# Kernel optimization log

Hardware: AMD Instinct MI355X
Metric: run time of the kernel (lower is better)

## Reference

```python
import jax, jax.numpy as jnp
from jax import lax
import numpy as np

EMBED, HIDDEN, VOCAB = 512, 512, 10000
ATT, ENC = 512, 2048
B, NPIX, T = 128, 49, 30


def _lin(k, out_d, in_d):
    k1, k2 = jax.random.split(k)
    s = 1.0 / np.sqrt(in_d)
    return (jax.random.uniform(k1, (out_d, in_d), minval=-s, maxval=s),
            jax.random.uniform(k2, (out_d,), minval=-s, maxval=s))


def setup_inputs() -> dict:
    key = jax.random.key(0)
    ks = jax.random.split(key, 24)
    inp = {}
    inp['enc_image'] = jax.random.normal(ks[0], (B, NPIX, ENC))
    inp['global_features'] = jax.random.normal(ks[1], (B, ENC))
    inp['encoded_captions'] = jax.random.randint(ks[2], (B, T), 0, VOCAB)
    lens = jax.random.randint(ks[3], (B,), 1, T + 1).at[0].set(T)
    inp['caption_lengths'] = lens[:, None]
    # parameters
    inp['emb_W'] = jax.random.uniform(ks[4], (VOCAB, EMBED), minval=-0.1, maxval=0.1)
    inp['e2h_W'], inp['e2h_b'] = _lin(ks[5], HIDDEN, ENC)
    inp['gf_W'], inp['gf_b'] = _lin(ks[6], EMBED, ENC)
    inp['fc_W'] = jax.random.uniform(ks[7], (VOCAB, HIDDEN), minval=-0.1, maxval=0.1)
    inp['fc_b'] = jnp.zeros((VOCAB,))
    inp['lstm_Wih'], inp['lstm_bih'] = _lin(ks[8], 4 * HIDDEN, 2 * EMBED)
    inp['lstm_Whh'], inp['lstm_bhh'] = _lin(ks[9], 4 * HIDDEN, HIDDEN)
    inp['xg_W'], inp['xg_b'] = _lin(ks[10], HIDDEN, 2 * EMBED)
    inp['hg_W'], inp['hg_b'] = _lin(ks[11], HIDDEN, HIDDEN)
    inp['senaff_W'], inp['senaff_b'] = _lin(ks[12], HIDDEN, HIDDEN)
    inp['senatt_W'], inp['senatt_b'] = _lin(ks[13], ATT, HIDDEN)
    inp['haff_W'], inp['haff_b'] = _lin(ks[14], HIDDEN, HIDDEN)
    inp['hatt_W'], inp['hatt_b'] = _lin(ks[15], ATT, HIDDEN)
    inp['vatt_W'], inp['vatt_b'] = _lin(ks[16], ATT, HIDDEN)
    inp['alph_W'], inp['alph_b'] = _lin(ks[17], 1, ATT)
    inp['ctx_W'], inp['ctx_b'] = _lin(ks[18], HIDDEN, HIDDEN)
    return inp


def reference(enc_image, global_features, encoded_captions, caption_lengths,
              emb_W, e2h_W, e2h_b, gf_W, gf_b, fc_W, fc_b,
              lstm_Wih, lstm_bih, lstm_Whh, lstm_bhh,
              xg_W, xg_b, hg_W, hg_b,
              senaff_W, senaff_b, senatt_W, senatt_b,
              haff_W, haff_b, hatt_W, hatt_b,
              vatt_W, vatt_b, alph_W, alph_b, ctx_W, ctx_b):
    lengths = caption_lengths[:, 0]
    order = jnp.argsort(-lengths)                     # descending (stable)
    lengths = lengths[order]
    spatial = jax.nn.relu(jnp.einsum('bpe,he->bph', enc_image[order], e2h_W) + e2h_b)  # (B,NP,H)
    gimg = jax.nn.relu(global_features[order] @ gf_W.T + gf_b)                          # (B,E)
    embs = emb_W[encoded_captions[order]]                                               # (B,T,E)
    inputs = jnp.concatenate([embs, jnp.broadcast_to(gimg[:, None, :], embs.shape)], axis=-1)  # (B,T,2E)
    vattn = jnp.einsum('bph,ah->bpa', spatial, vatt_W) + vatt_b                         # (B,NP,A) hoisted
    h0 = jnp.zeros((spatial.shape[0], HIDDEN), spatial.dtype)
    c0 = h0

    def step(carry, xs):
        h, c = carry
        xt, mask = xs                                  # (B,2E), (B,) bool = row still active
        gates = xt @ lstm_Wih.T + lstm_bih + h @ lstm_Whh.T + lstm_bhh
        i, f, g, o = jnp.split(gates, 4, axis=-1)
        c_new = jax.nn.sigmoid(f) * c + jax.nn.sigmoid(i) * jnp.tanh(g)
        h_new = jax.nn.sigmoid(o) * jnp.tanh(c_new)
        st = jax.nn.sigmoid(xt @ xg_W.T + xg_b + h @ hg_W.T + hg_b) * jnp.tanh(c_new)  # sentinel
        sen_aff = jax.nn.relu(st @ senaff_W.T + senaff_b)    # (B,H)
        sen_att = sen_aff @ senatt_W.T + senatt_b            # (B,A)
        h_aff = jnp.tanh(h_new @ haff_W.T + haff_b)
        h_att = h_aff @ hatt_W.T + hatt_b
        att_feats = jnp.concatenate([vattn, sen_att[:, None, :]], axis=1)   # (B,NP+1,A)
        scores = jnp.tanh(att_feats + h_att[:, None, :]) @ alph_W[0] + alph_b[0]
        alpha = jax.nn.softmax(scores, axis=1)               # (B,NP+1)
        cat_feats = jnp.concatenate([spatial, sen_aff[:, None, :]], axis=1)
        context = jnp.einsum('bph,bp->bh', cat_feats, alpha)
        out_l = jnp.tanh((context + h_aff) @ ctx_W.T + ctx_b)
        pt = out_l @ fc_W.T + fc_b                           # dropout = identity (eval)
        m = mask[:, None]
        return (jnp.where(m, h_new, h), jnp.where(m, c_new, c)), jnp.where(m, pt, 0.0)

    masks = lengths[None, :] > jnp.arange(T)[:, None]        # (T,B) replicates shrinking batch_size_t
    _, preds = lax.scan(step, (h0, c0), (jnp.swapaxes(inputs, 0, 1), masks))
    return jnp.swapaxes(preds, 0, 1)                         # (B,T,VOCAB), sorted-by-length order
```

## Files before the change

### kernel.cpp

```cpp
#include <hip/hip_runtime.h>
#include <hip/hip_bf16.h>
#include <cstdint>
#include <cstddef>

#define DEVI __device__ __forceinline__

#define BB 128
#define TT 30
#define VOCAB 10000
#define ENCD 2048
#define NPIX 49
#define SLOT 65536

typedef __attribute__((ext_vector_type(8))) short bf16x8;
typedef __attribute__((ext_vector_type(4))) float f32x4;

DEVI float bf2f(unsigned short u){ union{float f; unsigned int i;} x; x.i=((unsigned)u)<<16; return x.f; }
DEVI unsigned short f2bf(float f){ union{float f; unsigned int i;} x; x.f=f; unsigned r=x.i + 0x7fffu + ((x.i>>16)&1u); return (unsigned short)(r>>16); }
DEVI float sigm(float x){ return 1.0f/(1.0f+expf(-x)); }
DEVI f32x4 mfma16(bf16x8 a, bf16x8 b, f32x4 c){ return __builtin_amdgcn_mfma_f32_16x16x32_bf16(a,b,c,0,0,0); }

DEVI void gload_lds16(const void* g, void* l){
  __builtin_amdgcn_global_load_lds((const __attribute__((address_space(1))) unsigned int*)g,
                                   (__attribute__((address_space(3))) unsigned int*)l, 16, 0, 0);
}

DEVI void waitarr(int* base, int n, int thresh){
  __syncthreads();
  if(threadIdx.x < 64){
    for(;;){
      int v = (threadIdx.x<n) ? __hip_atomic_load(base + threadIdx.x*16, __ATOMIC_RELAXED, __HIP_MEMORY_SCOPE_AGENT)
                              : 0x7fffffff;
      if(__all(v >= thresh)) break;
      __builtin_amdgcn_s_sleep(8);
    }
  }
  asm volatile("" ::: "memory");
  __syncthreads();
}
DEVI void setflag(int* f, int val){
  __syncthreads();
  if(threadIdx.x==0) __hip_atomic_store(f, val, __ATOMIC_RELEASE, __HIP_MEMORY_SCOPE_AGENT);
}

__global__ void k_sort(const int* __restrict__ lens, int* __restrict__ order, int* __restrict__ Bt){
  __shared__ int L[BB];
  int i = threadIdx.x;
  L[i] = lens[i];
  __syncthreads();
  int li = L[i]; int rank = 0;
  for(int j=0;j<BB;j++){ int lj=L[j]; rank += (lj>li) || (lj==li && j<i); }
  order[rank] = i;
  if(i<TT){ int c=0; for(int j=0;j<BB;j++) c += (L[j]>i); Bt[i]=c; }
}

struct WC13 { const float* src[13]; unsigned short* dst[13]; int n[13]; };
__global__ void k_wconv(WC13 wc){
  int stride = gridDim.x*blockDim.x;
  int tid0 = blockIdx.x*blockDim.x + threadIdx.x;
  for(int s=0;s<13;s++){
    const float4* src=(const float4*)wc.src[s];
    int n4 = wc.n[s]>>2;
    ushort4* dst=(ushort4*)wc.dst[s];
    for(int i=tid0;i<n4;i+=stride){
      float4 v=src[i];
      ushort4 o; o.x=f2bf(v.x); o.y=f2bf(v.y); o.z=f2bf(v.z); o.w=f2bf(v.w);
      dst[i]=o;
    }
  }
}

__global__ void k_xt(const int* __restrict__ caps, const int* __restrict__ order,
                     const float* __restrict__ embW, const unsigned short* __restrict__ gimg,
                     unsigned short* __restrict__ xt){
  int total=BB*TT*1024;
  for(int idx=blockIdx.x*blockDim.x+threadIdx.x; idx<total; idx+=gridDim.x*blockDim.x){
    int k=idx&1023; int bt=idx>>10; int t=bt%TT; int b=bt/TT;
    unsigned short v;
    if(k<512){ int tok=caps[order[b]*TT+t]; v=f2bf(embW[(size_t)tok*512+k]); }
    else v=gimg[b*512+(k-512)];
    xt[idx]=v;
  }
}

__global__ __launch_bounds__(256) void k_gemm_f32A2(
    const float* __restrict__ A, int lda, int rpb, const int* __restrict__ order,
    const unsigned short* __restrict__ W, const float* __restrict__ bias,
    unsigned short* __restrict__ out, int K)
{
  __shared__ unsigned short As[128][136];
  int tid=threadIdx.x, wave=tid>>6, lane=tid&63, l15=lane&15, l4=lane>>4;
  int mb = blockIdx.y*128;
  f32x4 acc[8][4];
  f32x4 z = {0.f,0.f,0.f,0.f};
  #pragma unroll
  for(int i=0;i<8;i++)
    #pragma unroll
    for(int j=0;j<4;j++) acc[i][j]=z;
  int cch=tid&15, r0=tid>>4;
  int nb = blockIdx.x*256 + wave*64;
  for(int kc=0;kc<K;kc+=128){
    __syncthreads();
    #pragma unroll
    for(int rp=0;rp<8;rp++){
      int r=r0+rp*16;
      int m=mb+r;
      int sb = order[m/rpb]*rpb + m%rpb;
      const float* p = A + (size_t)sb*lda + kc + cch*8;
      float4 v0=*(const float4*)p, v1=*(const float4*)(p+4);
      unsigned short* d=&As[r][cch*8];
      d[0]=f2bf(v0.x); d[1]=f2bf(v0.y); d[2]=f2bf(v0.z); d[3]=f2bf(v0.w);
      d[4]=f2bf(v1.x); d[5]=f2bf(v1.y); d[6]=f2bf(v1.z); d[7]=f2bf(v1.w);
    }
    __syncthreads();
    #pragma unroll
    for(int kk=0;kk<4;kk++){
      bf16x8 bfr[4];
      #pragma unroll
      for(int nt=0;nt<4;nt++)
        bfr[nt] = *(const bf16x8*)(W + (size_t)(nb+nt*16+l15)*K + kc + kk*32 + l4*8);
      #pragma unroll
      for(int mt=0;mt<8;mt++){
        bf16x8 af = *(const bf16x8*)&As[mt*16+l15][kk*32+l4*8];
        #pragma unroll
        for(int nt=0;nt<4;nt++) acc[mt][nt]=mfma16(af,bfr[nt],acc[mt][nt]);
      }
    }
  }
  #pragma unroll
  for(int nt=0;nt<4;nt++){
    int n = nb + nt*16 + l15;
    float bs = bias[n];
    #pragma unroll
    for(int mt=0;mt<8;mt++){
      #pragma unroll
      for(int j=0;j<4;j++){
        int row = mb + mt*16 + l4*4 + j;
        float v = acc[mt][nt][j]+bs; v = v>0.f ? v : 0.f;
        out[(size_t)row*512 + n] = f2bf(v);
      }
    }
  }
}

DEVI void dev_gemm512c(unsigned short (*As)[136], const unsigned short* A, const unsigned short* W,
                       const float* bias, unsigned short* out, int xtile){
  int tid=threadIdx.x, wave=tid>>6, lane=tid&63, l15=lane&15, l4=lane>>4;
  f32x4 acc[8];
  f32x4 z = {0.f,0.f,0.f,0.f};
  #pragma unroll
  for(int i=0;i<8;i++) acc[i]=z;
  int cch=tid&15, r0=tid>>4;
  int nrow = xtile*64 + wave*16 + l15;
  for(int kc=0;kc<512;kc+=128){
    __syncthreads();
    #pragma unroll
    for(int rp=0;rp<8;rp++){
      int r=r0+rp*16;
      *(uint4*)&As[r][cch*8] = *(const uint4*)(A + (size_t)r*512 + kc + cch*8);
    }
    __syncthreads();
    #pragma unroll
    for(int kk=0;kk<4;kk++){
      bf16x8 bfr = *(const bf16x8*)(W + (size_t)nrow*512 + kc + kk*32 + l4*8);
      #pragma unroll
      for(int mt=0;mt<8;mt++){
        bf16x8 af = *(const bf16x8*)&As[mt*16+l15][kk*32+l4*8];
        acc[mt]=mfma16(af,bfr,acc[mt]);
      }
    }
  }
  float bs = bias ? bias[nrow] : 0.f;
  #pragma unroll
  for(int mt=0;mt<8;mt++){
    #pragma unroll
    for(int j=0;j<4;j++){
      int row = mt*16 + l4*4 + j;
      out[(size_t)row*512+nrow]=f2bf(acc[mt][j]+bs);
    }
  }
  __syncthreads();
}

struct PreD { const unsigned short* A; const unsigned short* W; const float* bias; unsigned short* out; };
struct PreD2 { PreD d[2]; };
__global__ __launch_bounds__(256) void k_pre(PreD2 dd){
  __shared__ unsigned short As[128][136];
  PreD g = dd.d[blockIdx.z];
  dev_gemm512c(As, g.A + (size_t)blockIdx.y*128*512, g.W, g.bias,
               g.out + (size_t)blockIdx.y*128*512, blockIdx.x);
}

__global__ __launch_bounds__(256) void k_gx(
    const unsigned short* __restrict__ xt, const unsigned short* __restrict__ w_ih,
    const unsigned short* __restrict__ w_xg,
    const float* __restrict__ bih, const float* __restrict__ bhh,
    const float* __restrict__ bxg, const float* __restrict__ bhg,
    unsigned short* __restrict__ Gx)
{
  __shared__ unsigned short As[128][136];
  int tid=threadIdx.x, wave=tid>>6, lane=tid&63, l15=lane&15, l4=lane>>4;
  int t = blockIdx.y;
  f32x4 acc[8];
  f32x4 z = {0.f,0.f,0.f,0.f};
  #pragma unroll
  for(int i=0;i<8;i++) acc[i]=z;
  int cch=tid&15, r0=tid>>4;
  int n = blockIdx.x*64 + wave*16 + l15;
  const unsigned short* wrow = (n<2048) ? (w_ih + (size_t)n*1024) : (w_xg + (size_t)(n-2048)*1024);
  for(int kc=0;kc<1024;kc+=128){
    __syncthreads();
    #pragma unroll
    for(int rp=0;rp<8;rp++){
      int r=r0+rp*16;
      *(uint4*)&As[r][cch*8] = *(const uint4*)(xt + (size_t)r*(TT*1024) + t*1024 + kc + cch*8);
    }
    __syncthreads();
    #pragma unroll
    for(int kk=0;kk<4;kk++){
      bf16x8 bfr = *(const bf16x8*)(wrow + kc + kk*32 + l4*8);
      #pragma unroll
      for(int mt=0;mt<8;mt++){
        bf16x8 af = *(const bf16x8*)&As[mt*16+l15][kk*32+l4*8];
        acc[mt]=mfma16(af,bfr,acc[mt]);
      }
    }
  }
  float bias = (n<2048) ? (bih[n]+bhh[n]) : (bxg[n-2048]+bhg[n-2048]);
  #pragma unroll
  for(int mt=0;mt<8;mt++){
    int row = mt*16 + l4*4;
    ushort4 o;
    o.x=f2bf(acc[mt][0]+bias); o.y=f2bf(acc[mt][1]+bias);
    o.z=f2bf(acc[mt][2]+bias); o.w=f2bf(acc[mt][3]+bias);
    *(ushort4*)(Gx + ((size_t)t*2560 + n)*128 + row) = o;
  }
}

struct PCtx {
  const unsigned short *w_hh, *w_hg, *Gx;
  const unsigned short *w_saff, *w_satt, *w_haff, *w_hatt, *w_ctx, *w_fc;
  const unsigned short *vattn, *SC;
  const float *sab,*stbias,*hab,*htb, *alW,*alb, *cxb, *fcb;
  const int *Bt;
  unsigned short *h_hist;
  unsigned short *stb;
  unsigned short *sbuf;
  float *dout;
  int *Lf,*SAf,*SBf,*S3f;
};

DEVI void stage_async(char* lds, const unsigned short* src){
  int wave = threadIdx.x>>6, lane = threadIdx.x&63;
  #pragma unroll
  for(int i=0;i<32;i++){
    int row = wave*32 + i;
    const unsigned short* g = src + (size_t)row*512 + ((lane ^ (row&7))<<3);
    gload_lds16(g, lds + row*1024 + lane*16);
  }
}
DEVI bf16x8 ldsA(const char* lds, int R, int cb){
  return *(const bf16x8*)(lds + R*1024 + (((unsigned)cb<<1) ^ ((unsigned)(R&7)<<4)));
}

DEVI void dev_lstmP(char* lds, const PCtx& p, int t, int cb,
                    const unsigned short* hprev, unsigned short* hout, float creg[2][4]){
  int tid=threadIdx.x, wave=tid>>6, lane=tid&63, l15=lane&15, l4=lane>>4;
  int jb = cb*16;
  int bt = p.Bt[t];
  __syncthreads();
  if(t>0) stage_async(lds, hprev);
  f32x4 acc[2][5];
  #pragma unroll
  for(int m=0;m<2;m++){
    #pragma unroll
    for(int s=0;s<5;s++){
      int col = (s<4) ? (s*512 + jb + l15) : (2048 + jb + l15);
      int row = (wave*2+m)*16 + l4*4;
      ushort4 g = *(const ushort4*)(p.Gx + ((size_t)t*2560 + col)*128 + row);
      acc[m][s][0]=bf2f(g.x); acc[m][s][1]=bf2f(g.y); acc[m][s][2]=bf2f(g.z); acc[m][s][3]=bf2f(g.w);
    }
  }
  __syncthreads();
  if(t>0){
    #pragma unroll
    for(int kk=0;kk<16;kk++){
      int kg = kk*32 + l4*8;
      bf16x8 bfr[5];
      #pragma unroll
      for(int s=0;s<5;s++){
        const unsigned short* wp = (s<4) ? (p.w_hh + (size_t)(s*512+jb+l15)*512 + kg)
                                         : (p.w_hg + (size_t)(jb+l15)*512 + kg);
        bfr[s] = *(const bf16x8*)wp;
      }
      #pragma unroll
      for(int m=0;m<2;m++){
        bf16x8 af = ldsA(lds, (wave*2+m)*16+l15, kk*32+l4*8);
        #pragma unroll
        for(int s=0;s<5;s++) acc[m][s]=mfma16(af,bfr[s],acc[m][s]);
      }
    }
  }
  int j = jb + l15;
  unsigned short* stt = p.stb + (size_t)t*SLOT;
  #pragma unroll
  for(int m=0;m<2;m++){
    int mt = wave*2+m;
    #pragma unroll
    for(int jj=0;jj<4;jj++){
      int b = mt*16 + l4*4 + jj;
      float iv = sigm(acc[m][0][jj]);
      float fv = sigm(acc[m][1][jj]);
      float gv = tanhf(acc[m][2][jj]);
      float ov = sigm(acc[m][3][jj]);
      float sv = sigm(acc[m][4][jj]);
      float cn = fv*creg[m][jj] + iv*gv;
      float tc = tanhf(cn);
      int hw = f2bf(ov*tc);
      int sw = f2bf(sv*tc);
      int hp = __shfl_xor(hw,1);
      int sp = __shfl_xor(sw,1);
      if(b<bt){
        if((l15&1)==0){
          *(unsigned*)(hout + (size_t)b*512 + j) = (unsigned)(hw&0xffff) | ((unsigned)hp<<16);
          *(unsigned*)(stt  + (size_t)b*512 + j) = (unsigned)(sw&0xffff) | ((unsigned)sp<<16);
        }
        creg[m][jj]=cn;
      }
    }
  }
}

DEVI void dev_mm1(char* lds, const unsigned short* src, const unsigned short* W,
                  const float* bias, unsigned short* out, int act, int xtile, int bt){
  int tid=threadIdx.x, wave=tid>>6, lane=tid&63, l15=lane&15, l4=lane>>4;
  __syncthreads();
  stage_async(lds, src);
  __syncthreads();
  int nrow = xtile*64 + wave*16 + l15;
  f32x4 acc[8];
  f32x4 z = {0.f,0.f,0.f,0.f};
  #pragma unroll
  for(int i=0;i<8;i++) acc[i]=z;
  #pragma unroll
  for(int kk=0;kk<16;kk++){
    bf16x8 bfr = *(const bf16x8*)(W + (size_t)nrow*512 + kk*32 + l4*8);
    #pragma unroll
    for(int mt=0;mt<8;mt++){
      bf16x8 af = ldsA(lds, mt*16+l15, kk*32+l4*8);
      acc[mt]=mfma16(af,bfr,acc[mt]);
    }
  }
  float bs = bias ? bias[nrow] : 0.f;
  #pragma unroll
  for(int mt=0;mt<8;mt++){
    #pragma unroll
    for(int j=0;j<4;j++){
      float v = acc[mt][j]+bs;
      if(act==1) v = fmaxf(v,0.f);
      else if(act==2) v = tanhf(v);
      int w = f2bf(v);
      int pw = __shfl_xor(w,1);
      int row = mt*16 + l4*4 + j;
      if((l15&1)==0 && row<bt)
        *(unsigned*)(out + (size_t)row*512 + (nrow&~1)) = (unsigned)(w&0xffff) | ((unsigned)pw<<16);
    }
  }
}

DEVI void dev_attn(float* sS, float* sA, unsigned short* sHA, unsigned short* sSA,
                   int b, const PCtx& p,
                   const unsigned short* satt, const unsigned short* hatt,
                   const unsigned short* scs, const unsigned short* sch,
                   unsigned short* outl){
  int tid=threadIdx.x;
  if(tid<64)       *(uint4*)&sHA[tid*8] = *(const uint4*)(hatt + (size_t)b*512 + tid*8);
  else if(tid<128){ int q=tid-64; *(uint4*)&sSA[q*8] = *(const uint4*)(satt + (size_t)b*512 + q*8); }
  __syncthreads();
  int gid=tid>>4, gl=tid&15;
  #pragma unroll
  for(int rp=0;rp<4;rp++){
    int pp = rp*16 + gid;
    float s = 0.f;
    if(pp<50){
      if(pp<NPIX){
        const unsigned short* vp = p.vattn + ((size_t)b*NPIX + pp)*512;
        #pragma unroll 8
        for(int k=gl*32;k<gl*32+32;k++) s += tanhf(bf2f(vp[k]) + bf2f(sHA[k])) * p.alW[k];
      } else {
        #pragma unroll 8
        for(int k=gl*32;k<gl*32+32;k++) s += tanhf(bf2f(sSA[k]) + bf2f(sHA[k])) * p.alW[k];
      }
    }
    #pragma unroll
    for(int off=8;off>=1;off>>=1) s += __shfl_xor(s, off);
    if(gl==0 && pp<50) sS[pp] = s + p.alb[0];
  }
  __syncthreads();
  if(tid<64){
    float sv = (tid<50) ? sS[tid] : -1e30f;
    float m = sv;
    #pragma unroll
    for(int off=32;off>=1;off>>=1) m = fmaxf(m, __shfl_xor(m, off));
    float e = (tid<50) ? expf(sv-m) : 0.f;
    float sum = e;
    #pragma unroll
    for(int off=32;off>=1;off>>=1) sum += __shfl_xor(sum, off);
    if(tid<50) sA[tid] = e/sum;
  }
  __syncthreads();
  float a49 = sA[49];
  {
    int n0 = tid*2;
    unsigned schU = *(const unsigned*)(sch + (size_t)b*512 + n0);
    unsigned scsU = *(const unsigned*)(scs + (size_t)b*512 + n0);
    float c0 = bf2f((unsigned short)schU), c1 = bf2f((unsigned short)(schU>>16));
    float s0 = bf2f((unsigned short)scsU), s1 = bf2f((unsigned short)(scsU>>16));
    float acc0 = c0 + a49*s0 + p.cxb[n0];
    float acc1 = c1 + a49*s1 + p.cxb[n0+1];
    const unsigned short* sp = p.SC + (size_t)b*NPIX*512 + n0;
    #pragma unroll 7
    for(int pp=0;pp<NPIX;pp++){
      unsigned u = *(const unsigned*)(sp + (size_t)pp*512);
      acc0 += sA[pp]*bf2f((unsigned short)u);
      acc1 += sA[pp]*bf2f((unsigned short)(u>>16));
    }
    unsigned o = ((unsigned)f2bf(tanhf(acc1))<<16) | (unsigned)(f2bf(tanhf(acc0))&0xffff);
    *(unsigned*)(outl + (size_t)b*512 + n0) = o;
  }
  __syncthreads();
}

DEVI void dev_fcF(char* lds, const PCtx& p, int t, int f, const unsigned short* outl){
  int tid=threadIdx.x;
  int bt = p.Bt[t];
  __syncthreads();
  stage_async(lds, outl);
  __syncthreads();
  int wave=tid>>6, lane=tid&63, l15=lane&15, l4=lane>>4;
  for(int x=f; x<157; x+=112){
    f32x4 acc[8];
    f32x4 z = {0.f,0.f,0.f,0.f};
    #pragma unroll
    for(int i=0;i<8;i++) acc[i]=z;
    int nbase = x*64 + wave*16;
    int nr = nbase + l15; if(nr > VOCAB-1) nr = VOCAB-1;
    #pragma unroll 4
    for(int kk=0;kk<16;kk++){
      bf16x8 bfr = *(const bf16x8*)(p.w_fc + (size_t)nr*512 + kk*32 + l4*8);
      #pragma unroll
      for(int mt=0;mt<8;mt++){
        if(mt*16 < bt){
          bf16x8 af = ldsA(lds, mt*16+l15, kk*32+l4*8);
          acc[mt]=mfma16(af,bfr,acc[mt]);
        }
      }
    }
    int n = nbase + l15; bool nok = n < VOCAB;
    float bs = nok ? p.fcb[n] : 0.f;
    #pragma unroll
    for(int mt=0;mt<8;mt++){
      #pragma unroll
      for(int j=0;j<4;j++){
        int b = mt*16 + l4*4 + j;
        float v = (b<bt) ? (acc[mt][j]+bs) : 0.f;
        if(nok) __builtin_nontemporal_store(v, &p.dout[(size_t)b*(TT*VOCAB) + (size_t)t*VOCAB + n]);
      }
    }
  }
}

__global__ __launch_bounds__(256) void k_persist(PCtx p){
  __shared__ __align__(16) char smem[133760];
  char* lds = smem;
  unsigned short* sHA = (unsigned short*)smem;
  unsigned short* sSA = sHA + 512;
  float* sS = (float*)(smem + 2048);
  float* sA = sS + 64;
  int cb = blockIdx.x;

  if(cb < 32){
    float creg[2][4];
    #pragma unroll
    for(int m=0;m<2;m++)
      #pragma unroll
      for(int j=0;j<4;j++) creg[m][j]=0.f;
    for(int t=0;t<TT;t++){
      if(t>0) waitarr(p.Lf, 32, t);
      dev_lstmP(lds, p, t, cb, p.h_hist + (size_t)t*SLOT, p.h_hist + (size_t)(t+1)*SLOT, creg);
      setflag(p.Lf + cb*16, t+1);
    }
  } else if(cb < 48){
    int w = cb-32;
    for(int t=0;t<TT;t++){
      waitarr(p.Lf, 32, t+1);
      int bt = p.Bt[t];
      unsigned short* S = p.sbuf + (size_t)t*7*SLOT;
      if(w<8) dev_mm1(lds, p.stb + (size_t)t*SLOT,        p.w_saff, p.sab, S,      1, w,   bt);
      else    dev_mm1(lds, p.h_hist + (size_t)(t+1)*SLOT, p.w_haff, p.hab, S+SLOT, 2, w-8, bt);
      setflag(p.SAf + w*16, t+1);
    }
  } else if(cb < 80){
    int w = cb-48;
    int q = w>>3, x0 = w&7;
    for(int t=0;t<TT;t++){
      waitarr(p.SAf, 16, t+1);
      int bt = p.Bt[t];
      unsigned short* S = p.sbuf + (size_t)t*7*SLOT;
      const unsigned short* src = (q==0||q==2) ? S : S+SLOT;
      const unsigned short* W   = (q==0)? p.w_satt : (q==1)? p.w_hatt : p.w_ctx;
      const float* bias         = (q==0)? p.stbias : (q==1)? p.htb    : nullptr;
      unsigned short* out       = S + (size_t)(2+q)*SLOT;
      dev_mm1(lds, src, W, bias, out, 0, x0, bt);
      setflag(p.SBf + w*16, t+1);
    }
  } else if(cb < 144){
    int w = cb-80;
    for(int t=0;t<TT;t++){
      waitarr(p.SBf, 32, t+1);
      int bt = p.Bt[t];
      unsigned short* S = p.sbuf + (size_t)t*7*SLOT;
      #pragma unroll
      for(int r=0;r<2;r++){
        int b = w*2+r;
        if(b < bt) dev_attn(sS,sA,sHA,sSA, b, p, S+2*SLOT, S+3*SLOT, S+4*SLOT, S+5*SLOT, S+6*SLOT);
      }
      setflag(p.S3f + w*16, t+1);
    }
  } else {
    int f = cb-144;
    for(int t=0;t<TT;t++){
      waitarr(p.S3f, 64, t+1);
      unsigned short* S = p.sbuf + (size_t)t*7*SLOT;
      dev_fcF(lds, p, t, f, S+6*SLOT);
    }
  }
}

extern "C" void kernel_launch(void* const* d_in, const int* in_sizes, int n_in,
                              void* d_out, int out_size, void* d_ws, size_t ws_size,
                              hipStream_t stream)
{
  const float* enc  =(const float*)d_in[0];
  const float* gfeat=(const float*)d_in[1];
  const int*   caps =(const int*)d_in[2];
  const int*   lens =(const int*)d_in[3];
  const float* embW =(const float*)d_in[4];
  const float* e2hW =(const float*)d_in[5];  const float* e2hb=(const float*)d_in[6];
  const float* gfW  =(const float*)d_in[7];  const float* gfb =(const float*)d_in[8];
  const float* fcW  =(const float*)d_in[9];  const float* fcb =(const float*)d_in[10];
  const float* WihF =(const float*)d_in[11]; const float* bih =(const float*)d_in[12];
  const float* WhhF =(const float*)d_in[13]; const float* bhh =(const float*)d_in[14];
  const float* xgWF =(const float*)d_in[15]; const float* bxg =(const float*)d_in[16];
  const float* hgWF =(const float*)d_in[17]; const float* bhg =(const float*)d_in[18];
  const float* saWF =(const float*)d_in[19]; const float* sab =(const float*)d_in[20];
  const float* stWF =(const float*)d_in[21]; const float* stbias=(const float*)d_in[22];
  const float* haWF =(const float*)d_in[23]; const float* hab =(const float*)d_in[24];
  const float* htWF =(const float*)d_in[25]; const float* htb =(const float*)d_in[26];
  const float* vaWF =(const float*)d_in[27]; const float* vab =(const float*)d_in[28];
  const float* alW  =(const float*)d_in[29]; const float* alb =(const float*)d_in[30];
  const float* cxWF =(const float*)d_in[31]; const float* cxb =(const float*)d_in[32];

  char* base=(char*)d_ws; size_t off=0;
  auto alloc=[&](size_t bytes)->void*{ void* r=base+off; off += (bytes+255)&~(size_t)255; return r; };

  int* order=(int*)alloc(BB*4);
  int* Bt   =(int*)alloc(32*4);
  unsigned short* w_e2h =(unsigned short*)alloc((size_t)512*2048*2);
  unsigned short* w_gf  =(unsigned short*)alloc((size_t)512*2048*2);
  unsigned short* w_fc  =(unsigned short*)alloc((size_t)VOCAB*512*2);
  unsigned short* w_ih  =(unsigned short*)alloc((size_t)2048*1024*2);
  unsigned short* w_hh  =(unsigned short*)alloc((size_t)2048*512*2);
  unsigned short* w_xg  =(unsigned short*)alloc((size_t)512*1024*2);
  unsigned short* w_hg  =(unsigned short*)alloc((size_t)512*512*2);
  unsigned short* w_saff=(unsigned short*)alloc((size_t)512*512*2);
  unsigned short* w_satt=(unsigned short*)alloc((size_t)512*512*2);
  unsigned short* w_haff=(unsigned short*)alloc((size_t)512*512*2);
  unsigned short* w_hatt=(unsigned short*)alloc((size_t)512*512*2);
  unsigned short* w_vatt=(unsigned short*)alloc((size_t)512*512*2);
  unsigned short* w_ctx =(unsigned short*)alloc((size_t)512*512*2);
  unsigned short* spatial=(unsigned short*)alloc((size_t)BB*NPIX*512*2);
  unsigned short* vattn  =(unsigned short*)alloc((size_t)BB*NPIX*512*2);
  unsigned short* SC     =(unsigned short*)alloc((size_t)BB*NPIX*512*2);
  unsigned short* gimg   =(unsigned short*)alloc((size_t)BB*512*2);
  unsigned short* xt     =(unsigned short*)alloc((size_t)BB*TT*1024*2);
  int* flags =(int*)alloc(16384);
  unsigned short* Gx  =(unsigned short*)alloc((size_t)TT*2560*128*2);
  unsigned short* sbuf=(unsigned short*)alloc((size_t)TT*7*SLOT*2);
  unsigned short* h_hist=(unsigned short*)alloc((size_t)(TT+1)*SLOT*2);
  unsigned short* stb_hist=(unsigned short*)alloc((size_t)TT*SLOT*2);

  k_sort<<<1,BB,0,stream>>>(lens, order, Bt);

  WC13 wc;
  const float* srcs[13] = {e2hW,gfW,fcW,WihF,WhhF,xgWF,hgWF,saWF,stWF,haWF,htWF,vaWF,cxWF};
  unsigned short* dsts[13] = {w_e2h,w_gf,w_fc,w_ih,w_hh,w_xg,w_hg,w_saff,w_satt,w_haff,w_hatt,w_vatt,w_ctx};
  int ns[13] = {512*2048,512*2048,VOCAB*512,2048*1024,2048*512,512*1024,512*512,512*512,512*512,512*512,512*512,512*512,512*512};
  for(int i=0;i<13;i++){ wc.src[i]=srcs[i]; wc.dst[i]=dsts[i]; wc.n[i]=ns[i]; }
  k_wconv<<<1024,256,0,stream>>>(wc);

  k_gemm_f32A2<<<dim3(2,NPIX),256,0,stream>>>(enc, ENCD, NPIX, order, w_e2h, e2hb, spatial, ENCD);
  k_gemm_f32A2<<<dim3(2,1),  256,0,stream>>>(gfeat, ENCD, 1, order, w_gf, gfb, gimg, ENCD);
  k_xt<<<1024,256,0,stream>>>(caps, order, embW, gimg, xt);
  {
    PreD2 dv{};
    dv.d[0] = PreD{spatial, w_vatt, vab,     vattn};
    dv.d[1] = PreD{spatial, w_ctx,  nullptr, SC};
    k_pre<<<dim3(8,NPIX,2),256,0,stream>>>(dv);
  }
  k_gx<<<dim3(40,TT),256,0,stream>>>(xt, w_ih, w_xg, bih, bhh, bxg, bhg, Gx);

  hipMemsetAsync(flags, 0, 16384, stream);

  PCtx pc;
  pc.w_hh=w_hh; pc.w_hg=w_hg; pc.Gx=Gx;
  pc.w_saff=w_saff; pc.w_satt=w_satt; pc.w_haff=w_haff; pc.w_hatt=w_hatt; pc.w_ctx=w_ctx; pc.w_fc=w_fc;
  pc.vattn=vattn; pc.SC=SC;
  pc.sab=sab; pc.stbias=stbias; pc.hab=hab; pc.htb=htb;
  pc.alW=alW; pc.alb=alb; pc.cxb=cxb; pc.fcb=fcb;
  pc.Bt=Bt;
  pc.h_hist=h_hist; pc.stb=stb_hist; pc.sbuf=sbuf;
  pc.dout=(float*)d_out;
  pc.Lf  = flags;
  pc.SAf = flags + 32*16;
  pc.SBf = flags + 48*16;
  pc.S3f = flags + 80*16;

  k_persist<<<256,256,0,stream>>>(pc);
}
```

Measured before the change: 2.656 ms.

## Consolidate persistent pipeline onto fewer blocks with multi-tile work per block

After: 8.743 ms. 3.29x slower.

```diff
diff --git a/kernel.cpp b/kernel.cpp
--- a/kernel.cpp
+++ b/kernel.cpp
@@ -24,7 +24,9 @@
   __builtin_amdgcn_global_load_lds((const __attribute__((address_space(1))) unsigned int*)g,
                                    (__attribute__((address_space(3))) unsigned int*)l, 16, 0, 0);
 }
-
+DEVI void nts4(unsigned short* p, unsigned v){ __builtin_nontemporal_store(v, (unsigned*)p); }
+
+template<int SLP>
 DEVI void waitarr(int* base, int n, int thresh){
   __syncthreads();
   if(threadIdx.x < 64){
@@ -32,7 +34,7 @@
       int v = (threadIdx.x<n) ? __hip_atomic_load(base + threadIdx.x*16, __ATOMIC_RELAXED, __HIP_MEMORY_SCOPE_AGENT)
                               : 0x7fffffff;
       if(__all(v >= thresh)) break;
-      __builtin_amdgcn_s_sleep(8);
+      __builtin_amdgcn_s_sleep(SLP);
     }
   }
   asm volatile("" ::: "memory");
@@ -263,107 +265,112 @@
   return *(const bf16x8*)(lds + R*1024 + (((unsigned)cb<<1) ^ ((unsigned)(R&7)<<4)));
 }
 
-DEVI void dev_lstmP(char* lds, const PCtx& p, int t, int cb,
-                    const unsigned short* hprev, unsigned short* hout, float creg[2][4]){
+DEVI void dev_lstmL(char* lds, const PCtx& p, int t, int cb,
+                    const unsigned short* hprev, unsigned short* hout, float creg[4][2][4]){
   int tid=threadIdx.x, wave=tid>>6, lane=tid&63, l15=lane&15, l4=lane>>4;
-  int jb = cb*16;
   int bt = p.Bt[t];
   __syncthreads();
   if(t>0) stage_async(lds, hprev);
-  f32x4 acc[2][5];
-  #pragma unroll
-  for(int m=0;m<2;m++){
-    #pragma unroll
-    for(int s=0;s<5;s++){
-      int col = (s<4) ? (s*512 + jb + l15) : (2048 + jb + l15);
-      int row = (wave*2+m)*16 + l4*4;
-      ushort4 g = *(const ushort4*)(p.Gx + ((size_t)t*2560 + col)*128 + row);
-      acc[m][s][0]=bf2f(g.x); acc[m][s][1]=bf2f(g.y); acc[m][s][2]=bf2f(g.z); acc[m][s][3]=bf2f(g.w);
-    }
-  }
-  __syncthreads();
-  if(t>0){
+  __syncthreads();
+  unsigned short* stt = p.stb + (size_t)t*SLOT;
+  #pragma unroll
+  for(int g=0;g<4;g++){
+    int jb = cb*64 + g*16;
+    f32x4 acc[2][5];
+    #pragma unroll
+    for(int m=0;m<2;m++){
+      #pragma unroll
+      for(int s=0;s<5;s++){
+        int col = (s<4) ? (s*512 + jb + l15) : (2048 + jb + l15);
+        int row = (wave*2+m)*16 + l4*4;
+        ushort4 gg = *(const ushort4*)(p.Gx + ((size_t)t*2560 + col)*128 + row);
+        acc[m][s][0]=bf2f(gg.x); acc[m][s][1]=bf2f(gg.y); acc[m][s][2]=bf2f(gg.z); acc[m][s][3]=bf2f(gg.w);
+      }
+    }
+    if(t>0){
+      #pragma unroll
+      for(int kk=0;kk<16;kk++){
+        int kg = kk*32 + l4*8;
+        bf16x8 bfr[5];
+        #pragma unroll
+        for(int s=0;s<5;s++){
+          const unsigned short* wp = (s<4) ? (p.w_hh + (size_t)(s*512+jb+l15)*512 + kg)
+                                           : (p.w_hg + (size_t)(jb+l15)*512 + kg);
+          bfr[s] = *(const bf16x8*)wp;
+        }
+        #pragma unroll
+        for(int m=0;m<2;m++){
+          bf16x8 af = ldsA(lds, (wave*2+m)*16+l15, kk*32+l4*8);
+          #pragma unroll
+          for(int s=0;s<5;s++) acc[m][s]=mfma16(af,bfr[s],acc[m][s]);
+        }
+      }
+    }
+    int j = jb + l15;
+    #pragma unroll
+    for(int m=0;m<2;m++){
+      int mt = wave*2+m;
+      #pragma unroll
+      for(int jj=0;jj<4;jj++){
+        int b = mt*16 + l4*4 + jj;
+        float iv = sigm(acc[m][0][jj]);
+        float fv = sigm(acc[m][1][jj]);
+        float gv = tanhf(acc[m][2][jj]);
+        float ov = sigm(acc[m][3][jj]);
+        float sv = sigm(acc[m][4][jj]);
+        float cn = fv*creg[g][m][jj] + iv*gv;
+        float tc = tanhf(cn);
+        int hw = f2bf(ov*tc);
+        int sw = f2bf(sv*tc);
+        int hp = __shfl_xor(hw,1);
+        int sp = __shfl_xor(sw,1);
+        if(b<bt){
+          if((l15&1)==0){
+            nts4(hout + (size_t)b*512 + j, (unsigned)(hw&0xffff) | ((unsigned)hp<<16));
+            nts4(stt  + (size_t)b*512 + j, (unsigned)(sw&0xffff) | ((unsigned)sp<<16));
+          }
+          creg[g][m][jj]=cn;
+        }
+      }
+    }
+  }
+}
+
+DEVI void dev_mmN(char* lds, const unsigned short* src, const unsigned short* W,
+                  const float* bias, unsigned short* out, int act, int x0, int ntiles, int bt){
+  int tid=threadIdx.x, wave=tid>>6, lane=tid&63, l15=lane&15, l4=lane>>4;
+  __syncthreads();
+  stage_async(lds, src);
+  __syncthreads();
+  for(int xi=0;xi<ntiles;xi++){
+    int nrow = (x0+xi)*64 + wave*16 + l15;
+    f32x4 acc[8];
+    f32x4 z = {0.f,0.f,0.f,0.f};
+    #pragma unroll
+    for(int i=0;i<8;i++) acc[i]=z;
     #pragma unroll
     for(int kk=0;kk<16;kk++){
-      int kg = kk*32 + l4*8;
-      bf16x8 bfr[5];
-      #pragma unroll
-      for(int s=0;s<5;s++){
-        const unsigned short* wp = (s<4) ? (p.w_hh + (size_t)(s*512+jb+l15)*512 + kg)
-                                         : (p.w_hg + (size_t)(jb+l15)*512 + kg);
-        bfr[s] = *(const bf16x8*)wp;
-      }
-      #pragma unroll
-      for(int m=0;m<2;m++){
-        bf16x8 af = ldsA(lds, (wave*2+m)*16+l15, kk*32+l4*8);
-        #pragma unroll
-        for(int s=0;s<5;s++) acc[m][s]=mfma16(af,bfr[s],acc[m][s]);
-      }
-    }
-  }
-  int j = jb + l15;
-  unsigned short* stt = p.stb + (size_t)t*SLOT;
-  #pragma unroll
-  for(int m=0;m<2;m++){
-    int mt = wave*2+m;
-    #pragma unroll
-    for(int jj=0;jj<4;jj++){
-      int b = mt*16 + l4*4 + jj;
-      float iv = sigm(acc[m][0][jj]);
-      float fv = sigm(acc[m][1][jj]);
-      float gv = tanhf(acc[m][2][jj]);
-      float ov = sigm(acc[m][3][jj]);
-      float sv = sigm(acc[m][4][jj]);
-      float cn = fv*creg[m][jj] + iv*gv;
-      float tc = tanhf(cn);
-      int hw = f2bf(ov*tc);
-      int sw = f2bf(sv*tc);
-      int hp = __shfl_xor(hw,1);
-      int sp = __shfl_xor(sw,1);
-      if(b<bt){
-        if((l15&1)==0){
-          *(unsigned*)(hout + (size_t)b*512 + j) = (unsigned)(hw&0xffff) | ((unsigned)hp<<16);
-          *(unsigned*)(stt  + (size_t)b*512 + j) = (unsigned)(sw&0xffff) | ((unsigned)sp<<16);
-        }
-        creg[m][jj]=cn;
-      }
-    }
-  }
-}
-
-DEVI void dev_mm1(char* lds, const unsigned short* src, const unsigned short* W,
-                  const float* bias, unsigned short* out, int act, int xtile, int bt){
-  int tid=threadIdx.x, wave=tid>>6, lane=tid&63, l15=lane&15, l4=lane>>4;
-  __syncthreads();
-  stage_async(lds, src);
-  __syncthreads();
-  int nrow = xtile*64 + wave*16 + l15;
-  f32x4 acc[8];
-  f32x4 z = {0.f,0.f,0.f,0.f};
-  #pragma unroll
-  for(int i=0;i<8;i++) acc[i]=z;
-  #pragma unroll
-  for(int kk=0;kk<16;kk++){
-    bf16x8 bfr = *(const bf16x8*)(W + (size_t)nrow*512 + kk*32 + l4*8);
+      bf16x8 bfr = *(const bf16x8*)(W + (size_t)nrow*512 + kk*32 + l4*8);
+      #pragma unroll
+      for(int mt=0;mt<8;mt++){
+        bf16x8 af = ldsA(lds, mt*16+l15, kk*32+l4*8);
+        acc[mt]=mfma16(af,bfr,acc[mt]);
+      }
+    }
+    float bs = bias ? bias[nrow] : 0.f;
     #pragma unroll
     for(int mt=0;mt<8;mt++){
-      bf16x8 af = ldsA(lds, mt*16+l15, kk*32+l4*8);
-      acc[mt]=mfma16(af,bfr,acc[mt]);
-    }
-  }
-  float bs = bias ? bias[nrow] : 0.f;
-  #pragma unroll
-  for(int mt=0;mt<8;mt++){
-    #pragma unroll
-    for(int j=0;j<4;j++){
-      float v = acc[mt][j]+bs;
-      if(act==1) v = fmaxf(v,0.f);
-      else if(act==2) v = tanhf(v);
-      int w = f2bf(v);
-      int pw = __shfl_xor(w,1);
-      int row = mt*16 + l4*4 + j;
-      if((l15&1)==0 && row<bt)
-        *(unsigned*)(out + (size_t)row*512 + (nrow&~1)) = (unsigned)(w&0xffff) | ((unsigned)pw<<16);
+      #pragma unroll
+      for(int j=0;j<4;j++){
+        float v = acc[mt][j]+bs;
+        if(act==1) v = fmaxf(v,0.f);
+        else if(act==2) v = tanhf(v);
+        int w = f2bf(v);
+        int pw = __shfl_xor(w,1);
+        int row = mt*16 + l4*4 + j;
+        if((l15&1)==0 && row<bt)
+          nts4(out + (size_t)row*512 + (nrow&~1), (unsigned)(w&0xffff) | ((unsigned)pw<<16));
+      }
     }
   }
 }
@@ -426,7 +433,7 @@
       acc1 += sA[pp]*bf2f((unsigned short)(u>>16));
     }
     unsigned o = ((unsigned)f2bf(tanhf(acc1))<<16) | (unsigned)(f2bf(tanhf(acc0))&0xffff);
-    *(unsigned*)(outl + (size_t)b*512 + n0) = o;
+    nts4(outl + (size_t)b*512 + n0, o);
   }
   __syncthreads();
 }
@@ -438,7 +445,7 @@
   stage_async(lds, outl);
   __syncthreads();
   int wave=tid>>6, lane=tid&63, l15=lane&15, l4=lane>>4;
-  for(int x=f; x<157; x+=112){
+  for(int x=f; x<157; x+=16){
     f32x4 acc[8];
     f32x4 z = {0.f,0.f,0.f,0.f};
     #pragma unroll
@@ -479,45 +486,47 @@
   float* sA = sS + 64;
   int cb = blockIdx.x;
 
-  if(cb < 32){
-    float creg[2][4];
-    #pragma unroll
-    for(int m=0;m<2;m++)
-      #pragma unroll
-      for(int j=0;j<4;j++) creg[m][j]=0.f;
+  if(cb < 8){
+    float creg[4][2][4];
+    #pragma unroll
+    for(int g=0;g<4;g++)
+      #pragma unroll
+      for(int m=0;m<2;m++)
+        #pragma unroll
+        for(int j=0;j<4;j++) creg[g][m][j]=0.f;
     for(int t=0;t<TT;t++){
-      if(t>0) waitarr(p.Lf, 32, t);
-      dev_lstmP(lds, p, t, cb, p.h_hist + (size_t)t*SLOT, p.h_hist + (size_t)(t+1)*SLOT, creg);
+      if(t>0) waitarr<4>(p.Lf, 8, t);
+      dev_lstmL(lds, p, t, cb, p.h_hist + (size_t)t*SLOT, p.h_hist + (size_t)(t+1)*SLOT, creg);
       setflag(p.Lf + cb*16, t+1);
     }
-  } else if(cb < 48){
-    int w = cb-32;
+  } else if(cb < 12){
+    int w = cb-8;
     for(int t=0;t<TT;t++){
-      waitarr(p.Lf, 32, t+1);
+      waitarr<32>(p.Lf, 8, t+1);
       int bt = p.Bt[t];
       unsigned short* S = p.sbuf + (size_t)t*7*SLOT;
-      if(w<8) dev_mm1(lds, p.stb + (size_t)t*SLOT,        p.w_saff, p.sab, S,      1, w,   bt);
-      else    dev_mm1(lds, p.h_hist + (size_t)(t+1)*SLOT, p.w_haff, p.hab, S+SLOT, 2, w-8, bt);
+      if(w<2) dev_mmN(lds, p.stb + (size_t)t*SLOT,        p.w_saff, p.sab, S,      1, w*4,     4, bt);
+      else    dev_mmN(lds, p.h_hist + (size_t)(t+1)*SLOT, p.w_haff, p.hab, S+SLOT, 2, (w-2)*4, 4, bt);
       setflag(p.SAf + w*16, t+1);
     }
-  } else if(cb < 80){
-    int w = cb-48;
-    int q = w>>3, x0 = w&7;
+  } else if(cb < 20){
+    int w = cb-12;
+    int q = w>>1, x0 = (w&1)*4;
     for(int t=0;t<TT;t++){
-      waitarr(p.SAf, 16, t+1);
+      waitarr<32>(p.SAf, 4, t+1);
       int bt = p.Bt[t];
       unsigned short* S = p.sbuf + (size_t)t*7*SLOT;
       const unsigned short* src = (q==0||q==2) ? S : S+SLOT;
       const unsigned short* W   = (q==0)? p.w_satt : (q==1)? p.w_hatt : p.w_ctx;
       const float* bias         = (q==0)? p.stbias : (q==1)? p.htb    : nullptr;
       unsigned short* out       = S + (size_t)(2+q)*SLOT;
-      dev_mm1(lds, src, W, bias, out, 0, x0, bt);
+      dev_mmN(lds, src, W, bias, out, 0, x0, 4, bt);
       setflag(p.SBf + w*16, t+1);
     }
-  } else if(cb < 144){
-    int w = cb-80;
+  } else if(cb < 84){
+    int w = cb-20;
     for(int t=0;t<TT;t++){
-      waitarr(p.SBf, 32, t+1);
+      waitarr<32>(p.SBf, 8, t+1);
       int bt = p.Bt[t];
       unsigned short* S = p.sbuf + (size_t)t*7*SLOT;
       #pragma unroll
@@ -528,9 +537,9 @@
       setflag(p.S3f + w*16, t+1);
     }
   } else {
-    int f = cb-144;
+    int f = cb-84;
     for(int t=0;t<TT;t++){
-      waitarr(p.S3f, 64, t+1);
+      waitarr<32>(p.S3f, 64, t+1);
       unsigned short* S = p.sbuf + (size_t)t*7*SLOT;
       dev_fcF(lds, p, t, f, S+6*SLOT);
     }
@@ -622,9 +631,9 @@
   pc.h_hist=h_hist; pc.stb=stb_hist; pc.sbuf=sbuf;
   pc.dout=(float*)d_out;
   pc.Lf  = flags;
-  pc.SAf = flags + 32*16;
-  pc.SBf = flags + 48*16;
-  pc.S3f = flags + 80*16;
-
-  k_persist<<<256,256,0,stream>>>(pc);
-}
+  pc.SAf = flags + 128;
+  pc.SBf = flags + 192;
+  pc.S3f = flags + 320;
+
+  k_persist<<<100,256,0,stream>>>(pc);
+}
```
